# Kernel tuning notes

Measured on AMD Instinct MI355X. Metric: run time of the kernel, lower is better.

The kernel has to match this reference:

```python
import jax, jax.numpy as jnp
import numpy as np

# dims: batch, channels, classes, transform channels, spatial
B, C, NCLS, T, H, W = 4, 512, 19, 256, 128, 128
NH, NW, PH, PW = 8, 8, 16, 16  # patch grid and patch size (H=NH*PH, no padding)


def conv1x1(x, w):
    # x: (b,c,h,w), w: (o,c) -> (b,o,h,w)
    return jnp.einsum('oc,bchw->bohw', w, x)


def conv3x3(x, w):
    return jax.lax.conv_general_dilated(x, w, (1, 1), 'SAME',
                                        dimension_numbers=('NCHW', 'OIHW', 'NCHW'))


def bn(x, s, b):
    # eval-mode BatchNorm folded into per-channel scale/shift
    return x * s[None, :, None, None] + b[None, :, None, None]


def relu6(x):
    return jnp.clip(x, 0.0, 6.0)


def patch_split(x):
    b, c = x.shape[0], x.shape[1]
    return x.reshape(b, c, NH, PH, NW, PW).transpose(0, 2, 4, 1, 3, 5).reshape(b * NH * NW, c, PH, PW)


def patch_recover(x):
    c = x.shape[1]
    return x.reshape(B, NH, NW, c, PH, PW).transpose(0, 3, 1, 4, 2, 5).reshape(B, c, H, W)


def setup_inputs() -> dict:
    key = jax.random.key(0)
    ks = jax.random.split(key, 40)

    def n(i, shape, s=1.0):
        return jax.random.normal(ks[i], shape, jnp.float32) * s

    def u(i, shape):
        return jax.random.uniform(ks[i], shape, jnp.float32, 0.5, 1.5)

    return {
        'feat': n(0, (B, C, H, W)),
        'global_center': n(1, (B, C, C), 1.0 / np.sqrt(C)),
        'w_proj': n(2, (C, C), 0.05), 'b_proj': n(3, (C,), 0.01),
        'w_dec': n(4, (NCLS, C), 0.05), 'b_dec': n(5, (NCLS,), 0.01),
        'q1_w': n(6, (T, C), 0.05), 'q1_s': u(7, (T,)), 'q1_b': n(8, (T,), 0.01),
        'q2_w': n(9, (T, T), 0.05), 'q2_s': u(10, (T,)), 'q2_b': n(11, (T,), 0.01),
        'k1_w': n(12, (T, C), 0.05), 'k1_s': u(13, (T,)), 'k1_b': n(14, (T,), 0.01),
        'k2_w': n(15, (T, T), 0.05), 'k2_s': u(16, (T,)), 'k2_b': n(17, (T,), 0.01),
        'v_w': n(18, (T, C), 0.05), 'v_s': u(19, (T,)), 'v_b': n(20, (T,), 0.01),
        'o_w': n(21, (C, T), 0.05), 'o_s': u(22, (C,)), 'o_b': n(23, (C,), 0.01),
        'cat1_w': n(24, (C, 2 * C, 3, 3), 0.02), 'cat1_s': u(25, (C,)), 'cat1_b': n(26, (C,), 0.01),
        'cat2_w': n(27, (C, C, 3, 3), 0.02), 'cat2_s': u(28, (C,)), 'cat2_b': n(29, (C,), 0.01),
    }


def reference(feat, global_center, w_proj, b_proj, w_dec, b_dec,
              q1_w, q1_s, q1_b, q2_w, q2_s, q2_b,
              k1_w, k1_s, k1_b, k2_w, k2_s, k2_b,
              v_w, v_s, v_b, o_w, o_s, o_b,
              cat1_w, cat1_s, cat1_b, cat2_w, cat2_s, cat2_b):
    relu = jax.nn.relu
    # class logits
    pred = conv1x1(feat, w_dec) + b_dec[None, :, None, None]          # (B,NCLS,H,W)
    residual = feat
    f = conv1x1(feat, w_proj) + b_proj[None, :, None, None]
    f = jnp.einsum('bcd,bdn->bcn', global_center, f.reshape(B, C, H * W)).reshape(B, C, H, W)
    f = relu6(residual + f)
    # patch split: N = B*NH*NW patches of (PH,PW)
    pf = patch_split(f)        # (N,C,PH,PW)
    pp = patch_split(pred)     # (N,NCLS,PH,PW)
    N = pf.shape[0]
    pp_flat = pp.reshape(N, NCLS, PH * PW)
    # LocalClassGatherModule (scale=1): per-class softmax over patch pixels
    probs = jax.nn.softmax(pp_flat, axis=2)                           # (N,NCLS,hw)
    ctx = jnp.einsum('nkp,ncp->nkc', probs, pf.reshape(N, C, PH * PW))  # (N,NCLS,C)
    # Recover: gather per-pixel class context via argmax label
    idx = jnp.argmax(pp_flat, axis=1)                                 # (N,hw)
    local = jnp.take_along_axis(ctx, idx[:, :, None], axis=1)         # (N,hw,C)
    local = local.transpose(0, 2, 1).reshape(N, C, PH, PW)
    # SelfAttentionBlock (correlate_net); BN in eval mode
    q = relu(bn(conv1x1(pf, q1_w), q1_s, q1_b))
    q = relu(bn(conv1x1(q, q2_w), q2_s, q2_b))
    k = relu(bn(conv1x1(local, k1_w), k1_s, k1_b))
    k = relu(bn(conv1x1(k, k2_w), k2_s, k2_b))
    v = relu(bn(conv1x1(local, v_w), v_s, v_b))
    qf = q.reshape(N, T, PH * PW).transpose(0, 2, 1)   # (N,hw,T)
    kf = k.reshape(N, T, PH * PW)                      # (N,T,hw)
    vf = v.reshape(N, T, PH * PW).transpose(0, 2, 1)   # (N,hw,T)
    sim = jax.nn.softmax(jnp.einsum('npt,ntq->npq', qf, kf) * T ** -0.5, axis=-1)
    cxt = jnp.einsum('npq,nqt->npt', sim, vf).transpose(0, 2, 1).reshape(N, T, PH, PW)
    cxt = relu(bn(conv1x1(cxt, o_w), o_s, o_b))        # (N,C,PH,PW)
    new_feat = patch_recover(cxt)                      # (B,C,H,W)
    # cat_conv (Dropout2d is identity in eval)
    out = jnp.concatenate([residual, new_feat], axis=1)
    out = relu6(bn(conv3x3(out, cat1_w), cat1_s, cat1_b))
    out = relu6(bn(conv3x3(out, cat2_w), cat2_s, cat2_b))
    return out
```

## Files before the change

kernel.cpp:

```cpp
#include <hip/hip_runtime.h>
#include <hip/hip_bf16.h>

typedef __attribute__((ext_vector_type(8))) short bf16x8;
typedef __attribute__((ext_vector_type(4))) float f32x4;

#define DEVFN __device__ __forceinline__

DEVFN float b2f(short s) {
    union { unsigned u; float f; } x;
    x.u = ((unsigned)(unsigned short)s) << 16;
    return x.f;
}
DEVFN unsigned short f2b(float f) {
    unsigned u = __float_as_uint(f);
    unsigned r = (u + 0x7FFFu + ((u >> 16) & 1u)) >> 16;
    return (unsigned short)r;
}

struct InPtrs { const void* p[27]; };

#define ARENA_TOT 1981976

__global__ void detect_k(const void* q1s, int* flag)
{
    const int ln = threadIdx.x;
    const unsigned short* s = (const unsigned short*)q1s;
    float v = b2f((short)s[ln]);
    int ok = (v >= 0.35f && v <= 1.7f) ? 1 : 0;
    for (int off = 32; off >= 1; off >>= 1) ok += __shfl_xor(ok, off, 64);
    if (ln == 0) *flag = (ok >= 56) ? 1 : 0;
}

__global__ __launch_bounds__(256) void cvt_arena(
    InPtrs ip, const int* __restrict__ flagp, unsigned short* __restrict__ arena)
{
    constexpr int SSZ[27] = {1048576,262144,512,9728,19,131072,256,256,65536,
        256,256,131072,256,256,65536,256,256,131072,256,256,131072,512,512,
        512,512,512,512};
    constexpr int SB[27] = {0,1048576,1310720,1311232,1320960,1320984,1452056,
        1452312,1452568,1518104,1518360,1518616,1649688,1649944,1650200,
        1715736,1715992,1716248,1847320,1847576,1847832,1978904,1979416,
        1979928,1980440,1980952,1981464};
    const int flag = *flagp;
    const int gid = blockIdx.x * 256 + threadIdx.x;
    const int stride = gridDim.x * 256;
    for (int s = 0; s < 27; ++s) {
        unsigned short* op = arena + SB[s];
        if (flag) {
            const unsigned short* in = (const unsigned short*)ip.p[s];
            for (int i = gid; i < SSZ[s]; i += stride) op[i] = in[i];
        } else {
            const float* in = (const float*)ip.p[s];
            for (int i = gid; i < SSZ[s]; i += stride) op[i] = f2b(in[i]);
        }
    }
}

__global__ __launch_bounds__(256) void feat_transpose(
    const void* __restrict__ in, const int* __restrict__ flagp,
    unsigned short* __restrict__ out)
{
    const int flag = *flagp;
    __shared__ unsigned short tile[64 * 65];
    const int tid = threadIdx.x;
    const int c0 = blockIdx.x * 64, r0 = blockIdx.y * 64;
    const size_t ibase = (size_t)blockIdx.z * 8388608;
    #pragma unroll
    for (int i = 0; i < 16; ++i) {
        int L = i * 256 + tid;
        int r = L >> 6, c = L & 63;
        size_t idx = ibase + (size_t)(r0 + r) * 16384 + c0 + c;
        tile[r * 65 + c] = flag ? ((const unsigned short*)in)[idx]
                                : f2b(((const float*)in)[idx]);
    }
    __syncthreads();
    #pragma unroll
    for (int i = 0; i < 16; ++i) {
        int L = i * 256 + tid;
        int cc = L >> 6, rr = L & 63;
        out[ibase + (size_t)(c0 + cc) * 512 + r0 + rr] = tile[rr * 65 + cc];
    }
}

__global__ __launch_bounds__(256) void transpose_k(
    const __hip_bfloat16* __restrict__ in, __hip_bfloat16* __restrict__ out,
    int R, int Cc)
{
    __shared__ __hip_bfloat16 tile[64 * 65];
    const int tid = threadIdx.x;
    const int c0 = blockIdx.x * 64, r0 = blockIdx.y * 64;
    #pragma unroll
    for (int i = 0; i < 16; ++i) {
        int L = i * 256 + tid;
        int r = L >> 6, c = L & 63;
        tile[r * 65 + c] = in[(size_t)(r0 + r) * Cc + c0 + c];
    }
    __syncthreads();
    #pragma unroll
    for (int i = 0; i < 16; ++i) {
        int L = i * 256 + tid;
        int cc = L >> 6, rr = L & 63;
        out[(size_t)(c0 + cc) * R + r0 + rr] = tile[rr * 65 + cc];
    }
}

__global__ void reorder_w(const void* __restrict__ w, const int* __restrict__ flagp,
                          unsigned short* __restrict__ wr, int CinN)
{
    const int flag = *flagp;
    int i = blockIdx.x * 256 + threadIdx.x;
    int total = 512 * CinN * 9;
    if (i >= total) return;
    int tap = i / (512 * CinN);
    int rem = i - tap * 512 * CinN;
    int o = rem / CinN;
    int c = rem - o * CinN;
    size_t si = ((size_t)o * CinN + c) * 9 + tap;
    wr[i] = flag ? ((const unsigned short*)w)[si] : f2b(((const float*)w)[si]);
}

__global__ void vb_k(const __hip_bfloat16* __restrict__ gc,
                     const __hip_bfloat16* __restrict__ bp,
                     float* __restrict__ vb)
{
    int i = blockIdx.x * 256 + threadIdx.x;
    const short* row = (const short*)gc + (size_t)i * 512;
    const short* bps = (const short*)bp;
    float a = 0.f;
    for (int d = 0; d < 512; ++d) a += b2f(row[d]) * b2f(bps[d]);
    vb[i] = a;
}

template <int EPI>
__global__ __launch_bounds__(256) void gemm_nt(
    const __hip_bfloat16* __restrict__ A, const __hip_bfloat16* __restrict__ Bw,
    __hip_bfloat16* __restrict__ Co, int K, int N,
    const __hip_bfloat16* __restrict__ sv, const __hip_bfloat16* __restrict__ bv,
    const float* __restrict__ vbp, const __hip_bfloat16* __restrict__ resid,
    long sA, long sB, long sC, int sV)
{
    __shared__ __hip_bfloat16 As[128 * 32];
    __shared__ __hip_bfloat16 Bs[128 * 32];
    const int tid = threadIdx.x;
    const int nb = blockIdx.x, mb = blockIdx.y, bz = blockIdx.z;
    A += (size_t)bz * sA;
    Bw += (size_t)bz * sB;
    Co += (size_t)bz * sC;
    if (EPI == 2) { resid += (size_t)bz * sC; vbp += (size_t)bz * (size_t)sV; }
    const int lane = tid & 63, wave = tid >> 6;
    const int wm = (wave >> 1) << 6, wn = (wave & 1) << 6;
    const int m15 = lane & 15, quad = lane >> 4;
    const int r0 = tid >> 2, koff = (tid & 3) << 3;
    f32x4 acc[4][4];
    #pragma unroll
    for (int i = 0; i < 4; ++i)
        #pragma unroll
        for (int j = 0; j < 4; ++j) {
            acc[i][j][0] = 0.f; acc[i][j][1] = 0.f;
            acc[i][j][2] = 0.f; acc[i][j][3] = 0.f;
        }
    const size_t abase = (size_t)(mb * 128 + r0) * K + koff;
    const size_t bbase = (size_t)(nb * 128 + r0) * K + koff;
    for (int k0 = 0; k0 < K; k0 += 32) {
        bf16x8 a0 = *(const bf16x8*)(A + abase + k0);
        bf16x8 a1 = *(const bf16x8*)(A + abase + (size_t)64 * K + k0);
        bf16x8 b0 = *(const bf16x8*)(Bw + bbase + k0);
        bf16x8 b1 = *(const bf16x8*)(Bw + bbase + (size_t)64 * K + k0);
        __syncthreads();
        *(bf16x8*)&As[r0 * 32 + koff] = a0;
        *(bf16x8*)&As[(r0 + 64) * 32 + koff] = a1;
        *(bf16x8*)&Bs[r0 * 32 + koff] = b0;
        *(bf16x8*)&Bs[(r0 + 64) * 32 + koff] = b1;
        __syncthreads();
        bf16x8 af[4], bfv[4];
        #pragma unroll
        for (int mt = 0; mt < 4; ++mt)
            af[mt] = *(const bf16x8*)&As[(wm + mt * 16 + m15) * 32 + quad * 8];
        #pragma unroll
        for (int nt = 0; nt < 4; ++nt)
            bfv[nt] = *(const bf16x8*)&Bs[(wn + nt * 16 + m15) * 32 + quad * 8];
        #pragma unroll
        for (int mt = 0; mt < 4; ++mt)
            #pragma unroll
            for (int nt = 0; nt < 4; ++nt)
                acc[mt][nt] = __builtin_amdgcn_mfma_f32_16x16x32_bf16(
                    af[mt], bfv[nt], acc[mt][nt], 0, 0, 0);
    }
    unsigned short* outp = (unsigned short*)Co;
    #pragma unroll
    for (int nt = 0; nt < 4; ++nt) {
        const int n = nb * 128 + wn + nt * 16 + m15;
        float sc = 0.f, sh = 0.f, vbn = 0.f;
        if (EPI == 1) { sc = b2f(((const short*)sv)[n]); sh = b2f(((const short*)bv)[n]); }
        if (EPI == 2) vbn = vbp[n];
        #pragma unroll
        for (int mt = 0; mt < 4; ++mt) {
            const int mb2 = mb * 128 + wm + mt * 16 + quad * 4;
            #pragma unroll
            for (int r = 0; r < 4; ++r) {
                const int m = mb2 + r;
                float v = acc[mt][nt][r];
                if (EPI == 1) {
                    v = fmaxf(v * sc + sh, 0.f);
                } else if (EPI == 2) {
                    v += vbn + b2f(((const short*)resid)[(size_t)m * N + n]);
                    v = fminf(fmaxf(v, 0.f), 6.f);
                }
                outp[(size_t)m * N + n] = f2b(v);
            }
        }
    }
}

template <int CIN, bool CHMAJOR>
__global__ __launch_bounds__(256) void conv3x3k(
    const __hip_bfloat16* __restrict__ in0, const __hip_bfloat16* __restrict__ in1,
    const __hip_bfloat16* __restrict__ Wt, void* __restrict__ outp,
    const __hip_bfloat16* __restrict__ sv, const __hip_bfloat16* __restrict__ bv,
    const int* __restrict__ flagp)
{
    __shared__ __hip_bfloat16 smem[128 * 144];
    __hip_bfloat16* As = smem;
    __hip_bfloat16* Bs = smem + 4096;
    const int tid = threadIdx.x;
    const int nb = blockIdx.x, h = blockIdx.y, b = blockIdx.z;
    const int lane = tid & 63, wave = tid >> 6;
    const int wm = (wave >> 1) << 6, wn = (wave & 1) << 6;
    const int m15 = lane & 15, quad = lane >> 4;
    const int r0 = tid >> 2, koff = (tid & 3) << 3;
    f32x4 acc[4][4];
    #pragma unroll
    for (int i = 0; i < 4; ++i)
        #pragma unroll
        for (int j = 0; j < 4; ++j) {
            acc[i][j][0] = 0.f; acc[i][j][1] = 0.f;
            acc[i][j][2] = 0.f; acc[i][j][3] = 0.f;
        }
    const size_t pixbase = (size_t)b * 16384 + (size_t)h * 128;
    for (int tap = 0; tap < 9; ++tap) {
        const int dy = tap / 3 - 1, dx = tap % 3 - 1;
        const int hh = h + dy;
        const bool hok = (unsigned)hh < 128u;
        const __hip_bfloat16* wtap = Wt + (size_t)tap * 512 * CIN;
        const size_t rowbase = (size_t)b * 16384 + (size_t)hh * 128;
        for (int c0 = 0; c0 < CIN; c0 += 32) {
            const __hip_bfloat16* src = (CIN > 512 && c0 >= 512) ? in1 : in0;
            const int cl = c0 & 511;
            bf16x8 a0, a1, b0, b1;
            {
                int ww = r0 + dx;
                if (hok && (unsigned)ww < 128u)
                    a0 = *(const bf16x8*)&src[(rowbase + ww) * 512 + cl + koff];
                else
                    for (int j = 0; j < 8; ++j) a0[j] = 0;
                ww = r0 + 64 + dx;
                if (hok && (unsigned)ww < 128u)
                    a1 = *(const bf16x8*)&src[(rowbase + ww) * 512 + cl + koff];
                else
                    for (int j = 0; j < 8; ++j) a1[j] = 0;
            }
            b0 = *(const bf16x8*)&wtap[(size_t)(nb * 128 + r0) * CIN + c0 + koff];
            b1 = *(const bf16x8*)&wtap[(size_t)(nb * 128 + r0 + 64) * CIN + c0 + koff];
            __syncthreads();
            *(bf16x8*)&As[r0 * 32 + koff] = a0;
            *(bf16x8*)&As[(r0 + 64) * 32 + koff] = a1;
            *(bf16x8*)&Bs[r0 * 32 + koff] = b0;
            *(bf16x8*)&Bs[(r0 + 64) * 32 + koff] = b1;
            __syncthreads();
            bf16x8 af[4], bfv[4];
            #pragma unroll
            for (int mt = 0; mt < 4; ++mt)
                af[mt] = *(const bf16x8*)&As[(wm + mt * 16 + m15) * 32 + quad * 8];
            #pragma unroll
            for (int nt = 0; nt < 4; ++nt)
                bfv[nt] = *(const bf16x8*)&Bs[(wn + nt * 16 + m15) * 32 + quad * 8];
            #pragma unroll
            for (int mt = 0; mt < 4; ++mt)
                #pragma unroll
                for (int nt = 0; nt < 4; ++nt)
                    acc[mt][nt] = __builtin_amdgcn_mfma_f32_16x16x32_bf16(
                        af[mt], bfv[nt], acc[mt][nt], 0, 0, 0);
        }
    }
    if (!CHMAJOR) {
        unsigned short* op = (unsigned short*)outp;
        #pragma unroll
        for (int nt = 0; nt < 4; ++nt) {
            const int n = nb * 128 + wn + nt * 16 + m15;
            const float sc = b2f(((const short*)sv)[n]);
            const float sh = b2f(((const short*)bv)[n]);
            #pragma unroll
            for (int mt = 0; mt < 4; ++mt) {
                #pragma unroll
                for (int r = 0; r < 4; ++r) {
                    const int wc = wm + mt * 16 + quad * 4 + r;
                    float v = fminf(fmaxf(acc[mt][nt][r] * sc + sh, 0.f), 6.f);
                    op[(pixbase + wc) * 512 + n] = f2b(v);
                }
            }
        }
    } else {
        __syncthreads();
        unsigned short* sm16 = (unsigned short*)smem;
        #pragma unroll
        for (int nt = 0; nt < 4; ++nt) {
            const int nloc = wn + nt * 16 + m15;
            const int n = nb * 128 + nloc;
            const float sc = b2f(((const short*)sv)[n]);
            const float sh = b2f(((const short*)bv)[n]);
            #pragma unroll
            for (int mt = 0; mt < 4; ++mt) {
                #pragma unroll
                for (int r = 0; r < 4; ++r) {
                    const int wc = wm + mt * 16 + quad * 4 + r;
                    float v = fminf(fmaxf(acc[mt][nt][r] * sc + sh, 0.f), 6.f);
                    sm16[nloc * 144 + wc] = f2b(v);
                }
            }
        }
        __syncthreads();
        const int flag = *flagp;
        const int nr = tid >> 1, half = (tid & 1) * 64;
        const size_t gbase = ((size_t)(b * 512 + nb * 128 + nr)) * 16384 +
                             (size_t)h * 128 + half;
        const unsigned short* srow = sm16 + nr * 144 + half;
        if (flag) {
            unsigned short* oh = (unsigned short*)outp;
            #pragma unroll
            for (int j = 0; j < 8; ++j)
                *(bf16x8*)&oh[gbase + j * 8] = *(const bf16x8*)&srow[j * 8];
        } else {
            float* of = (float*)outp;
            #pragma unroll
            for (int j = 0; j < 64; j += 4) {
                f32x4 v;
                v[0] = b2f((short)srow[j]);
                v[1] = b2f((short)srow[j + 1]);
                v[2] = b2f((short)srow[j + 2]);
                v[3] = b2f((short)srow[j + 3]);
                *(f32x4*)&of[gbase + j] = v;
            }
        }
    }
}

__global__ __launch_bounds__(256) void patch_pred(
    const __hip_bfloat16* __restrict__ featT, const __hip_bfloat16* __restrict__ f2T,
    const __hip_bfloat16* __restrict__ w_dec, const __hip_bfloat16* __restrict__ b_dec,
    float* __restrict__ ctx_g, int* __restrict__ cnt_g)
{
    __shared__ __hip_bfloat16 wds[19 * 512];
    __shared__ float pp[19 * 256];
    __shared__ int cnt[19];
    const int tid = threadIdx.x;
    const int n = blockIdx.x;
    const int b = n >> 6, nh = (n >> 3) & 7, nw = n & 7;
    const int ph = tid >> 4, pw = tid & 15;
    const size_t pbase = (size_t)b * 16384 + (size_t)nh * 2048 + (size_t)nw * 16;
    const size_t g = pbase + (size_t)ph * 128 + pw;
    if (tid < 19) cnt[tid] = 0;
    for (int i = tid; i < 19 * 512; i += 256) wds[i] = w_dec[i];
    __syncthreads();
    float lg[19];
    #pragma unroll
    for (int k = 0; k < 19; ++k) lg[k] = b2f(((const short*)b_dec)[k]);
    const __hip_bfloat16* xrow = featT + g * 512;
    for (int c0 = 0; c0 < 512; c0 += 8) {
        bf16x8 x8 = *(const bf16x8*)&xrow[c0];
        float xf[8];
        #pragma unroll
        for (int j = 0; j < 8; ++j) xf[j] = b2f(x8[j]);
        #pragma unroll
        for (int k = 0; k < 19; ++k) {
            bf16x8 w8 = *(const bf16x8*)&wds[k * 512 + c0];
            #pragma unroll
            for (int j = 0; j < 8; ++j) lg[k] += xf[j] * b2f(w8[j]);
        }
    }
    int best = 0;
    float bvv = lg[0];
    #pragma unroll
    for (int k = 1; k < 19; ++k)
        if (lg[k] > bvv) { bvv = lg[k]; best = k; }
    atomicAdd(&cnt[best], 1);
    #pragma unroll
    for (int k = 0; k < 19; ++k) pp[k * 256 + tid] = lg[k];
    __syncthreads();
    if (tid < 19) cnt_g[n * 19 + tid] = cnt[tid];
    const int wv = tid >> 6, ln = tid & 63;
    for (int k = wv; k < 19; k += 4) {
        float v0 = pp[k * 256 + ln], v1 = pp[k * 256 + 64 + ln];
        float v2 = pp[k * 256 + 128 + ln], v3 = pp[k * 256 + 192 + ln];
        float mx = fmaxf(fmaxf(v0, v1), fmaxf(v2, v3));
        for (int off = 32; off >= 1; off >>= 1) mx = fmaxf(mx, __shfl_xor(mx, off, 64));
        float e0 = __expf(v0 - mx), e1 = __expf(v1 - mx);
        float e2 = __expf(v2 - mx), e3 = __expf(v3 - mx);
        float s = e0 + e1 + e2 + e3;
        for (int off = 32; off >= 1; off >>= 1) s += __shfl_xor(s, off, 64);
        float inv = 1.f / s;
        pp[k * 256 + ln] = e0 * inv;
        pp[k * 256 + 64 + ln] = e1 * inv;
        pp[k * 256 + 128 + ln] = e2 * inv;
        pp[k * 256 + 192 + ln] = e3 * inv;
    }
    __syncthreads();
    const short* f2s = (const short*)f2T;
    for (int o = tid; o < 19 * 512; o += 256) {
        const int k = o >> 9, c = o & 511;
        const short* p0 = f2s + pbase * 512 + c;
        const float* ppk = &pp[k * 256];
        float a = 0.f;
        for (int pr = 0; pr < 16; ++pr) {
            const short* prow = p0 + (size_t)pr * 65536;
            const float* ppr = ppk + pr * 16;
            #pragma unroll
            for (int pc = 0; pc < 16; ++pc)
                a += ppr[pc] * b2f(prow[(size_t)pc * 512]);
        }
        ctx_g[(size_t)n * 9728 + o] = a;
    }
}

__global__ __launch_bounds__(256) void patch_kv(
    const float* __restrict__ ctx_g,
    const __hip_bfloat16* __restrict__ k1w, const __hip_bfloat16* __restrict__ k1s,
    const __hip_bfloat16* __restrict__ k1b,
    const __hip_bfloat16* __restrict__ k2w, const __hip_bfloat16* __restrict__ k2s,
    const __hip_bfloat16* __restrict__ k2b,
    const __hip_bfloat16* __restrict__ vw, const __hip_bfloat16* __restrict__ vs,
    const __hip_bfloat16* __restrict__ vbq,
    const __hip_bfloat16* __restrict__ ow,
    float* __restrict__ k2c_g, float* __restrict__ OV_g)
{
    __shared__ float ctx_s[19 * 512];
    __shared__ float tmp_s[256 * 20];
    const int tid = threadIdx.x;
    const int n = blockIdx.x;
    for (int i = tid; i < 19 * 512; i += 256) ctx_s[i] = ctx_g[(size_t)n * 9728 + i];
    __syncthreads();
    const int t = tid;
    float a[19];
    #pragma unroll
    for (int k = 0; k < 19; ++k) a[k] = 0.f;
    for (int c0 = 0; c0 < 512; c0 += 8) {
        bf16x8 w8 = *(const bf16x8*)&k1w[t * 512 + c0];
        float wf[8];
        #pragma unroll
        for (int j = 0; j < 8; ++j) wf[j] = b2f(w8[j]);
        #pragma unroll
        for (int k = 0; k < 19; ++k) {
            f32x4 ca = *(const f32x4*)&ctx_s[k * 512 + c0];
            f32x4 cb = *(const f32x4*)&ctx_s[k * 512 + c0 + 4];
            a[k] += wf[0]*ca[0] + wf[1]*ca[1] + wf[2]*ca[2] + wf[3]*ca[3]
                  + wf[4]*cb[0] + wf[5]*cb[1] + wf[6]*cb[2] + wf[7]*cb[3];
        }
    }
    {
        float sc = b2f(((const short*)k1s)[t]), sh = b2f(((const short*)k1b)[t]);
        #pragma unroll
        for (int k = 0; k < 19; ++k) tmp_s[t * 20 + k] = fmaxf(a[k] * sc + sh, 0.f);
    }
    __syncthreads();
    #pragma unroll
    for (int k = 0; k < 19; ++k) a[k] = 0.f;
    for (int t0 = 0; t0 < 256; t0 += 8) {
        bf16x8 w8 = *(const bf16x8*)&k2w[t * 256 + t0];
        #pragma unroll
        for (int j = 0; j < 8; ++j) {
            float wf = b2f(w8[j]);
            #pragma unroll
            for (int k = 0; k < 19; ++k) a[k] += wf * tmp_s[(t0 + j) * 20 + k];
        }
    }
    {
        float sc = b2f(((const short*)k2s)[t]), sh = b2f(((const short*)k2b)[t]);
        #pragma unroll
        for (int k = 0; k < 19; ++k)
            k2c_g[((size_t)n * 256 + t) * 19 + k] = fmaxf(a[k] * sc + sh, 0.f);
    }
    __syncthreads();
    #pragma unroll
    for (int k = 0; k < 19; ++k) a[k] = 0.f;
    for (int c0 = 0; c0 < 512; c0 += 8) {
        bf16x8 w8 = *(const bf16x8*)&vw[t * 512 + c0];
        float wf[8];
        #pragma unroll
        for (int j = 0; j < 8; ++j) wf[j] = b2f(w8[j]);
        #pragma unroll
        for (int k = 0; k < 19; ++k) {
            f32x4 ca = *(const f32x4*)&ctx_s[k * 512 + c0];
            f32x4 cb = *(const f32x4*)&ctx_s[k * 512 + c0 + 4];
            a[k] += wf[0]*ca[0] + wf[1]*ca[1] + wf[2]*ca[2] + wf[3]*ca[3]
                  + wf[4]*cb[0] + wf[5]*cb[1] + wf[6]*cb[2] + wf[7]*cb[3];
        }
    }
    {
        float sc = b2f(((const short*)vs)[t]), sh = b2f(((const short*)vbq)[t]);
        #pragma unroll
        for (int k = 0; k < 19; ++k) tmp_s[t * 20 + k] = fmaxf(a[k] * sc + sh, 0.f);
    }
    __syncthreads();
    for (int cc = t; cc < 512; cc += 256) {
        float o[19];
        #pragma unroll
        for (int k = 0; k < 19; ++k) o[k] = 0.f;
        for (int t0 = 0; t0 < 256; t0 += 8) {
            bf16x8 w8 = *(const bf16x8*)&ow[cc * 256 + t0];
            #pragma unroll
            for (int j = 0; j < 8; ++j) {
                float wf = b2f(w8[j]);
                #pragma unroll
                for (int k = 0; k < 19; ++k) o[k] += wf * tmp_s[(t0 + j) * 20 + k];
            }
        }
        #pragma unroll
        for (int k = 0; k < 19; ++k) OV_g[((size_t)n * 512 + cc) * 19 + k] = o[k];
    }
}

__global__ __launch_bounds__(256) void patch_attn(
    const __hip_bfloat16* __restrict__ qT, const float* __restrict__ k2c_g,
    const float* __restrict__ OV_g, const int* __restrict__ cnt_g,
    const __hip_bfloat16* __restrict__ os, const __hip_bfloat16* __restrict__ ob,
    __hip_bfloat16* __restrict__ nfT)
{
    __shared__ float k2s[256 * 19];
    __shared__ float OVs[512 * 19];
    __shared__ float osf[512], obf[512];
    __shared__ int cnts[19];
    const int tid = threadIdx.x;
    const int n = blockIdx.x;
    const int b = n >> 6, nh = (n >> 3) & 7, nw = n & 7;
    const int ph = tid >> 4, pw = tid & 15;
    const size_t g = (size_t)b * 16384 + (size_t)(nh * 16 + ph) * 128 + (nw * 16 + pw);
    for (int i = tid; i < 4864; i += 256) k2s[i] = k2c_g[(size_t)n * 4864 + i];
    for (int i = tid; i < 9728; i += 256) OVs[i] = OV_g[(size_t)n * 9728 + i];
    for (int i = tid; i < 512; i += 256) {
        osf[i] = b2f(((const short*)os)[i]);
        obf[i] = b2f(((const short*)ob)[i]);
    }
    if (tid < 19) cnts[tid] = cnt_g[n * 19 + tid];
    __syncthreads();
    float L[19];
    #pragma unroll
    for (int k = 0; k < 19; ++k) L[k] = 0.f;
    const short* qrow = (const short*)qT + g * 256;
    for (int t0 = 0; t0 < 256; t0 += 8) {
        bf16x8 q8 = *(const bf16x8*)&qrow[t0];
        #pragma unroll
        for (int j = 0; j < 8; ++j) {
            float qj = b2f(q8[j]);
            #pragma unroll
            for (int k = 0; k < 19; ++k) L[k] += qj * k2s[(t0 + j) * 19 + k];
        }
    }
    #pragma unroll
    for (int k = 0; k < 19; ++k) L[k] *= 0.0625f;
    float m = -1e30f;
    #pragma unroll
    for (int k = 0; k < 19; ++k)
        if (cnts[k] > 0) m = fmaxf(m, L[k]);
    float wgt[19], Z = 0.f;
    #pragma unroll
    for (int k = 0; k < 19; ++k) {
        float e = (cnts[k] > 0) ? (float)cnts[k] * __expf(L[k] - m) : 0.f;
        wgt[k] = e;
        Z += e;
    }
    float iz = 1.f / Z;
    #pragma unroll
    for (int k = 0; k < 19; ++k) wgt[k] *= iz;
    unsigned short* orow = (unsigned short*)nfT + g * 512;
    for (int c = 0; c < 512; c += 2) {
        float v0 = 0.f, v1 = 0.f;
        #pragma unroll
        for (int k = 0; k < 19; ++k) {
            v0 += wgt[k] * OVs[c * 19 + k];
            v1 += wgt[k] * OVs[(c + 1) * 19 + k];
        }
        v0 = fmaxf(osf[c] * v0 + obf[c], 0.f);
        v1 = fmaxf(osf[c + 1] * v1 + obf[c + 1], 0.f);
        unsigned pack = (unsigned)f2b(v0) | ((unsigned)f2b(v1) << 16);
        *(unsigned*)&orow[c] = pack;
    }
}

extern "C" void kernel_launch(void* const* d_in, const int* in_sizes, int n_in,
                              void* d_out, int out_size, void* d_ws, size_t ws_size,
                              hipStream_t stream)
{
    (void)in_sizes; (void)n_in; (void)out_size; (void)ws_size;

    char* ws = (char*)d_ws;
    constexpr size_t MiB = 1024ul * 1024;
    constexpr size_t O_W0   = 0;
    constexpr size_t O_W1   = 64 * MiB;
    constexpr size_t O_W2   = 96 * MiB;
    constexpr size_t O_w1r  = 128 * MiB;
    constexpr size_t O_w2r  = O_w1r + 9ul * 512 * 1024 * 2;
    constexpr size_t O_wpT  = O_w2r + 9ul * 512 * 512 * 2;
    constexpr size_t O_Mm   = O_wpT + 512ul * 512 * 2;
    constexpr size_t O_vb   = O_Mm + 4ul * 512 * 512 * 2;
    constexpr size_t O_ctx  = O_vb + 8192;
    constexpr size_t O_cnt  = O_ctx + 256ul * 19 * 512 * 4;
    constexpr size_t O_ar   = O_cnt + 32768;
    constexpr size_t O_flag = O_ar + (size_t)ARENA_TOT * 2;

    unsigned short* arena = (unsigned short*)(ws + O_ar);
    int*            flag  = (int*)(ws + O_flag);
    __hip_bfloat16* featT = (__hip_bfloat16*)d_out;
    __hip_bfloat16* f2T   = (__hip_bfloat16*)(ws + O_W0);
    __hip_bfloat16* nfT   = (__hip_bfloat16*)(ws + O_W0);
    __hip_bfloat16* q1T   = (__hip_bfloat16*)(ws + O_W1);
    float*          k2c   = (float*)(ws + O_W1);
    float*          OV    = (float*)(ws + O_W1 + 256ul * 256 * 19 * 4);
    __hip_bfloat16* c1T   = (__hip_bfloat16*)(ws + O_W1);
    __hip_bfloat16* qT    = (__hip_bfloat16*)(ws + O_W2);
    unsigned short* w1r   = (unsigned short*)(ws + O_w1r);
    unsigned short* w2r   = (unsigned short*)(ws + O_w2r);
    __hip_bfloat16* wpT   = (__hip_bfloat16*)(ws + O_wpT);
    __hip_bfloat16* Mmat  = (__hip_bfloat16*)(ws + O_Mm);
    float*          vb    = (float*)(ws + O_vb);
    float*          ctx   = (float*)(ws + O_ctx);
    int*            cnt   = (int*)(ws + O_cnt);

    const int AB_gc = 0, AB_wproj = 1048576, AB_bproj = 1310720,
        AB_wdec = 1311232, AB_bdec = 1320960, AB_q1w = 1320984,
        AB_q1s = 1452056, AB_q1b = 1452312, AB_q2w = 1452568,
        AB_q2s = 1518104, AB_q2b = 1518360, AB_k1w = 1518616,
        AB_k1s = 1649688, AB_k1b = 1649944, AB_k2w = 1650200,
        AB_k2s = 1715736, AB_k2b = 1715992, AB_vw = 1716248,
        AB_vs = 1847320, AB_vb = 1847576, AB_ow = 1847832,
        AB_os = 1978904, AB_ob = 1979416, AB_c1s = 1979928,
        AB_c1b = 1980440, AB_c2s = 1980952, AB_c2b = 1981464;
    #define AR(off) ((__hip_bfloat16*)(arena + (off)))

    InPtrs ip;
    {
        const int idx[27] = {1,2,3,4,5,6,7,8,9,10,11,12,13,14,15,16,17,18,19,
                             20,21,22,23,25,26,28,29};
        for (int i = 0; i < 27; ++i) ip.p[i] = d_in[idx[i]];
    }

    detect_k<<<dim3(1), 64, 0, stream>>>(d_in[7], flag);
    cvt_arena<<<dim3(1024), 256, 0, stream>>>(ip, flag, arena);
    feat_transpose<<<dim3(256, 8, 4), 256, 0, stream>>>(d_in[0], flag,
                                                        (unsigned short*)featT);
    transpose_k<<<dim3(8, 8, 1), 256, 0, stream>>>(AR(AB_wproj), wpT, 512, 512);
    reorder_w<<<dim3((512 * 1024 * 9 + 255) / 256), 256, 0, stream>>>(
        d_in[24], flag, w1r, 1024);
    reorder_w<<<dim3((512 * 512 * 9 + 255) / 256), 256, 0, stream>>>(
        d_in[27], flag, w2r, 512);
    vb_k<<<dim3(8), 256, 0, stream>>>(AR(AB_gc), AR(AB_bproj), vb);
    gemm_nt<0><<<dim3(4, 4, 4), 256, 0, stream>>>(
        AR(AB_gc), wpT, Mmat, 512, 512, nullptr, nullptr, nullptr, nullptr,
        512L * 512, 0L, 512L * 512, 0);
    gemm_nt<2><<<dim3(4, 128, 4), 256, 0, stream>>>(
        featT, Mmat, f2T, 512, 512, nullptr, nullptr, vb, featT,
        16384L * 512, 512L * 512, 16384L * 512, 512);
    patch_pred<<<dim3(256), 256, 0, stream>>>(featT, f2T, AR(AB_wdec),
                                              AR(AB_bdec), ctx, cnt);
    gemm_nt<1><<<dim3(2, 512, 1), 256, 0, stream>>>(
        f2T, AR(AB_q1w), q1T, 512, 256, AR(AB_q1s), AR(AB_q1b),
        nullptr, nullptr, 0L, 0L, 0L, 0);
    gemm_nt<1><<<dim3(2, 512, 1), 256, 0, stream>>>(
        q1T, AR(AB_q2w), qT, 256, 256, AR(AB_q2s), AR(AB_q2b),
        nullptr, nullptr, 0L, 0L, 0L, 0);
    patch_kv<<<dim3(256), 256, 0, stream>>>(
        ctx, AR(AB_k1w), AR(AB_k1s), AR(AB_k1b), AR(AB_k2w), AR(AB_k2s),
        AR(AB_k2b), AR(AB_vw), AR(AB_vs), AR(AB_vb), AR(AB_ow), k2c, OV);
    patch_attn<<<dim3(256), 256, 0, stream>>>(qT, k2c, OV, cnt, AR(AB_os),
                                              AR(AB_ob), nfT);
    conv3x3k<1024, false><<<dim3(4, 128, 4), 256, 0, stream>>>(
        featT, nfT, (const __hip_bfloat16*)w1r, c1T, AR(AB_c1s), AR(AB_c1b), flag);
    conv3x3k<512, true><<<dim3(4, 128, 4), 256, 0, stream>>>(
        c1T, c1T, (const __hip_bfloat16*)w2r, d_out, AR(AB_c2s), AR(AB_c2b), flag);
}
```

Measured before the change: 2.247 ms.

## Use direct global-to-LDS loads with XOR swizzle and XCD-aware conv block mapping

GEMM and conv3x3 kernels now stage weight (and GEMM activation) tiles with global_load_lds 16-byte direct loads into LDS using an XOR-swizzled layout, and the fragment reads use the matching swizzle to cut bank conflicts. The conv kernels switch to a 1D grid remapped so each XCD handles a contiguous band of image rows, aiming for better L2 reuse of halo rows. The channel-major epilogue is split into two halves to shrink the LDS footprint to 8448 elements, which may raise occupancy. Risks include correctness of the swizzle and LDS-direct load layout, plus extra barriers in the epilogue.

```diff
diff --git a/kernel.cpp b/kernel.cpp
--- a/kernel.cpp
+++ b/kernel.cpp
@@ -15,6 +15,11 @@
     unsigned u = __float_as_uint(f);
     unsigned r = (u + 0x7FFFu + ((u >> 16) & 1u)) >> 16;
     return (unsigned short)r;
+}
+DEVFN void gload16(const __hip_bfloat16* g, __hip_bfloat16* l) {
+    __builtin_amdgcn_global_load_lds(
+        (const __attribute__((address_space(1))) void*)g,
+        (__attribute__((address_space(3))) void*)l, 16, 0, 0);
 }
 
 struct InPtrs { const void* p[27]; };
@@ -139,8 +144,8 @@
     const float* __restrict__ vbp, const __hip_bfloat16* __restrict__ resid,
     long sA, long sB, long sC, int sV)
 {
-    __shared__ __hip_bfloat16 As[128 * 32];
-    __shared__ __hip_bfloat16 Bs[128 * 32];
+    __shared__ __hip_bfloat16 As[4096];
+    __shared__ __hip_bfloat16 Bs[4096];
     const int tid = threadIdx.x;
     const int nb = blockIdx.x, mb = blockIdx.y, bz = blockIdx.z;
     A += (size_t)bz * sA;
@@ -150,7 +155,9 @@
     const int lane = tid & 63, wave = tid >> 6;
     const int wm = (wave >> 1) << 6, wn = (wave & 1) << 6;
     const int m15 = lane & 15, quad = lane >> 4;
-    const int r0 = tid >> 2, koff = (tid & 3) << 3;
+    const int srow = lane >> 2;
+    const int sgoff = ((lane & 3) ^ ((lane >> 2) & 3) ^ ((lane >> 4) & 3)) * 8;
+    const int fsw = (quad ^ (m15 & 3) ^ ((m15 >> 2) & 3)) * 8;
     f32x4 acc[4][4];
     #pragma unroll
     for (int i = 0; i < 4; ++i)
@@ -159,26 +166,25 @@
             acc[i][j][0] = 0.f; acc[i][j][1] = 0.f;
             acc[i][j][2] = 0.f; acc[i][j][3] = 0.f;
         }
-    const size_t abase = (size_t)(mb * 128 + r0) * K + koff;
-    const size_t bbase = (size_t)(nb * 128 + r0) * K + koff;
+    const size_t abase = (size_t)mb * 128 * K;
+    const size_t bbase = (size_t)nb * 128 * K;
     for (int k0 = 0; k0 < K; k0 += 32) {
-        bf16x8 a0 = *(const bf16x8*)(A + abase + k0);
-        bf16x8 a1 = *(const bf16x8*)(A + abase + (size_t)64 * K + k0);
-        bf16x8 b0 = *(const bf16x8*)(Bw + bbase + k0);
-        bf16x8 b1 = *(const bf16x8*)(Bw + bbase + (size_t)64 * K + k0);
         __syncthreads();
-        *(bf16x8*)&As[r0 * 32 + koff] = a0;
-        *(bf16x8*)&As[(r0 + 64) * 32 + koff] = a1;
-        *(bf16x8*)&Bs[r0 * 32 + koff] = b0;
-        *(bf16x8*)&Bs[(r0 + 64) * 32 + koff] = b1;
+        #pragma unroll
+        for (int j = 0; j < 2; ++j) {
+            const int i = wave * 2 + j;
+            const int row = i * 16 + srow;
+            gload16(A + abase + (size_t)row * K + k0 + sgoff, &As[i * 512]);
+            gload16(Bw + bbase + (size_t)row * K + k0 + sgoff, &Bs[i * 512]);
+        }
         __syncthreads();
         bf16x8 af[4], bfv[4];
         #pragma unroll
         for (int mt = 0; mt < 4; ++mt)
-            af[mt] = *(const bf16x8*)&As[(wm + mt * 16 + m15) * 32 + quad * 8];
+            af[mt] = *(const bf16x8*)&As[(wm + mt * 16 + m15) * 32 + fsw];
         #pragma unroll
         for (int nt = 0; nt < 4; ++nt)
-            bfv[nt] = *(const bf16x8*)&Bs[(wn + nt * 16 + m15) * 32 + quad * 8];
+            bfv[nt] = *(const bf16x8*)&Bs[(wn + nt * 16 + m15) * 32 + fsw];
         #pragma unroll
         for (int mt = 0; mt < 4; ++mt)
             #pragma unroll
@@ -219,15 +225,24 @@
     const __hip_bfloat16* __restrict__ sv, const __hip_bfloat16* __restrict__ bv,
     const int* __restrict__ flagp)
 {
-    __shared__ __hip_bfloat16 smem[128 * 144];
+    __shared__ __hip_bfloat16 smem[8448];
     __hip_bfloat16* As = smem;
     __hip_bfloat16* Bs = smem + 4096;
     const int tid = threadIdx.x;
-    const int nb = blockIdx.x, h = blockIdx.y, b = blockIdx.z;
+    const int L = blockIdx.x;
+    const int xcd = L & 7;
+    const int g = L >> 3;
+    const int nb = g & 3;
+    const int h = xcd * 16 + ((g >> 2) & 15);
+    const int b = g >> 6;
     const int lane = tid & 63, wave = tid >> 6;
     const int wm = (wave >> 1) << 6, wn = (wave & 1) << 6;
     const int m15 = lane & 15, quad = lane >> 4;
-    const int r0 = tid >> 2, koff = (tid & 3) << 3;
+    const int r0 = tid >> 2, akoff = (tid & 3) << 3;
+    const int asw = (((tid & 3) ^ ((tid >> 2) & 3) ^ ((tid >> 4) & 3))) * 8;
+    const int srow = lane >> 2;
+    const int sgoff = ((lane & 3) ^ ((lane >> 2) & 3) ^ ((lane >> 4) & 3)) * 8;
+    const int fsw = (quad ^ (m15 & 3) ^ ((m15 >> 2) & 3)) * 8;
     f32x4 acc[4][4];
     #pragma unroll
     for (int i = 0; i < 4; ++i)
@@ -246,34 +261,37 @@
         for (int c0 = 0; c0 < CIN; c0 += 32) {
             const __hip_bfloat16* src = (CIN > 512 && c0 >= 512) ? in1 : in0;
             const int cl = c0 & 511;
-            bf16x8 a0, a1, b0, b1;
+            bf16x8 a0, a1;
             {
                 int ww = r0 + dx;
                 if (hok && (unsigned)ww < 128u)
-                    a0 = *(const bf16x8*)&src[(rowbase + ww) * 512 + cl + koff];
+                    a0 = *(const bf16x8*)&src[(rowbase + ww) * 512 + cl + akoff];
                 else
                     for (int j = 0; j < 8; ++j) a0[j] = 0;
                 ww = r0 + 64 + dx;
                 if (hok && (unsigned)ww < 128u)
-                    a1 = *(const bf16x8*)&src[(rowbase + ww) * 512 + cl + koff];
+                    a1 = *(const bf16x8*)&src[(rowbase + ww) * 512 + cl + akoff];
                 else
                     for (int j = 0; j < 8; ++j) a1[j] = 0;
             }
-            b0 = *(const bf16x8*)&wtap[(size_t)(nb * 128 + r0) * CIN + c0 + koff];
-            b1 = *(const bf16x8*)&wtap[(size_t)(nb * 128 + r0 + 64) * CIN + c0 + koff];
             __syncthreads();
-            *(bf16x8*)&As[r0 * 32 + koff] = a0;
-            *(bf16x8*)&As[(r0 + 64) * 32 + koff] = a1;
-            *(bf16x8*)&Bs[r0 * 32 + koff] = b0;
-            *(bf16x8*)&Bs[(r0 + 64) * 32 + koff] = b1;
+            #pragma unroll
+            for (int j = 0; j < 2; ++j) {
+                const int i = wave * 2 + j;
+                const int row = i * 16 + srow;
+                gload16(wtap + (size_t)(nb * 128 + row) * CIN + c0 + sgoff,
+                        &Bs[i * 512]);
+            }
+            *(bf16x8*)&As[r0 * 32 + asw] = a0;
+            *(bf16x8*)&As[(r0 + 64) * 32 + asw] = a1;
             __syncthreads();
             bf16x8 af[4], bfv[4];
             #pragma unroll
             for (int mt = 0; mt < 4; ++mt)
-                af[mt] = *(const bf16x8*)&As[(wm + mt * 16 + m15) * 32 + quad * 8];
+                af[mt] = *(const bf16x8*)&As[(wm + mt * 16 + m15) * 32 + fsw];
             #pragma unroll
             for (int nt = 0; nt < 4; ++nt)
-                bfv[nt] = *(const bf16x8*)&Bs[(wn + nt * 16 + m15) * 32 + quad * 8];
+                bfv[nt] = *(const bf16x8*)&Bs[(wn + nt * 16 + m15) * 32 + fsw];
             #pragma unroll
             for (int mt = 0; mt < 4; ++mt)
                 #pragma unroll
@@ -300,46 +318,53 @@
             }
         }
     } else {
+        const int flag = *flagp;
+        unsigned short* sm16 = (unsigned short*)smem;
         __syncthreads();
-        unsigned short* sm16 = (unsigned short*)smem;
-        #pragma unroll
-        for (int nt = 0; nt < 4; ++nt) {
-            const int nloc = wn + nt * 16 + m15;
-            const int n = nb * 128 + nloc;
-            const float sc = b2f(((const short*)sv)[n]);
-            const float sh = b2f(((const short*)bv)[n]);
-            #pragma unroll
-            for (int mt = 0; mt < 4; ++mt) {
+        #pragma unroll
+        for (int half = 0; half < 2; ++half) {
+            if ((wn >> 6) == half) {
                 #pragma unroll
-                for (int r = 0; r < 4; ++r) {
-                    const int wc = wm + mt * 16 + quad * 4 + r;
-                    float v = fminf(fmaxf(acc[mt][nt][r] * sc + sh, 0.f), 6.f);
-                    sm16[nloc * 144 + wc] = f2b(v);
+                for (int nt = 0; nt < 4; ++nt) {
+                    const int nl = nt * 16 + m15;
+                    const int n = nb * 128 + half * 64 + nl;
+                    const float sc = b2f(((const short*)sv)[n]);
+                    const float sh = b2f(((const short*)bv)[n]);
+                    #pragma unroll
+                    for (int mt = 0; mt < 4; ++mt) {
+                        #pragma unroll
+                        for (int r = 0; r < 4; ++r) {
+                            const int wc = wm + mt * 16 + quad * 4 + r;
+                            float v = fminf(fmaxf(acc[mt][nt][r] * sc + sh, 0.f), 6.f);
+                            sm16[nl * 130 + wc] = f2b(v);
+                        }
+                    }
                 }
             }
-        }
-        __syncthreads();
-        const int flag = *flagp;
-        const int nr = tid >> 1, half = (tid & 1) * 64;
-        const size_t gbase = ((size_t)(b * 512 + nb * 128 + nr)) * 16384 +
-                             (size_t)h * 128 + half;
-        const unsigned short* srow = sm16 + nr * 144 + half;
-        if (flag) {
-            unsigned short* oh = (unsigned short*)outp;
-            #pragma unroll
-            for (int j = 0; j < 8; ++j)
-                *(bf16x8*)&oh[gbase + j * 8] = *(const bf16x8*)&srow[j * 8];
-        } else {
-            float* of = (float*)outp;
-            #pragma unroll
-            for (int j = 0; j < 64; j += 4) {
-                f32x4 v;
-                v[0] = b2f((short)srow[j]);
-                v[1] = b2f((short)srow[j + 1]);
-                v[2] = b2f((short)srow[j + 2]);
-                v[3] = b2f((short)srow[j + 3]);
-                *(f32x4*)&of[gbase + j] = v;
+            __syncthreads();
+            const int nr = tid >> 2, qt = tid & 3;
+            const int och = nb * 128 + half * 64 + nr;
+            const size_t gb = ((size_t)(b * 512 + och)) * 16384 +
+                              (size_t)h * 128 + qt * 32;
+            const unsigned short* srw = sm16 + nr * 130 + qt * 32;
+            if (flag) {
+                unsigned short* oh = (unsigned short*)outp;
+                #pragma unroll
+                for (int j = 0; j < 4; ++j)
+                    *(bf16x8*)&oh[gb + j * 8] = *(const bf16x8*)&srw[j * 8];
+            } else {
+                float* of = (float*)outp;
+                #pragma unroll
+                for (int j = 0; j < 32; j += 4) {
+                    f32x4 v;
+                    v[0] = b2f((short)srw[j]);
+                    v[1] = b2f((short)srw[j + 1]);
+                    v[2] = b2f((short)srw[j + 2]);
+                    v[3] = b2f((short)srw[j + 3]);
+                    *(f32x4*)&of[gb + j] = v;
+                }
             }
+            __syncthreads();
         }
     }
 }
@@ -671,8 +696,8 @@
         AR(AB_k2b), AR(AB_vw), AR(AB_vs), AR(AB_vb), AR(AB_ow), k2c, OV);
     patch_attn<<<dim3(256), 256, 0, stream>>>(qT, k2c, OV, cnt, AR(AB_os),
                                               AR(AB_ob), nfT);
-    conv3x3k<1024, false><<<dim3(4, 128, 4), 256, 0, stream>>>(
+    conv3x3k<1024, false><<<dim3(2048), 256, 0, stream>>>(
         featT, nfT, (const __hip_bfloat16*)w1r, c1T, AR(AB_c1s), AR(AB_c1b), flag);
-    conv3x3k<512, true><<<dim3(4, 128, 4), 256, 0, stream>>>(
+    conv3x3k<512, true><<<dim3(2048), 256, 0, stream>>>(
         c1T, c1T, (const __hip_bfloat16*)w2r, d_out, AR(AB_c2s), AR(AB_c2b), flag);
 }
```

After: 2.115 ms. 5.9% less time.
